# Optimization experiments

Measured on AMD Instinct MI355X. Metric: run time of the kernel, lower is better.

Reference implementation:

```python
import jax, jax.numpy as jnp
import numpy as np

BN_EPS = 1e-5

def batch_norm(x, gamma, beta):
    # training-mode BatchNorm1d: biased batch stats over the edge dim
    mean = jnp.mean(x, axis=0)
    var = jnp.var(x, axis=0)
    return (x - mean) * jax.lax.rsqrt(var + BN_EPS) * gamma + beta

def setup_inputs() -> dict:
    key = jax.random.key(0)
    ks = jax.random.split(key, 10)
    N, F, E = 50000, 128, 600000
    D_in = 2 * F + 12  # 268
    h = jax.random.normal(ks[0], (N, F), dtype=jnp.float32)
    edge_feature = jax.random.normal(ks[1], (E, 12), dtype=jnp.float32)
    src = jax.random.randint(ks[2], (E,), 0, N)
    dst = jax.random.randint(ks[3], (E,), 0, N)
    def lin(k, fan_in, shape):
        bound = 1.0 / np.sqrt(fan_in)
        return jax.random.uniform(k, shape, jnp.float32, -bound, bound)
    W1 = lin(ks[4], D_in, (28, D_in)); b1 = lin(ks[5], D_in, (28,))
    W2 = lin(ks[6], 28, (8, 28));      b2 = lin(ks[7], 28, (8,))
    W3 = lin(ks[8], 8, (1, 8));        b3 = lin(ks[9], 8, (1,))
    gamma1 = jnp.ones((28,), jnp.float32); beta1 = jnp.zeros((28,), jnp.float32)
    gamma2 = jnp.ones((8,), jnp.float32);  beta2 = jnp.zeros((8,), jnp.float32)
    return {"h": h, "edge_feature": edge_feature, "src": src, "dst": dst,
            "W1": W1, "b1": b1, "gamma1": gamma1, "beta1": beta1,
            "W2": W2, "b2": b2, "gamma2": gamma2, "beta2": beta2,
            "W3": W3, "b3": b3}

def reference(h, edge_feature, src, dst, W1, b1, gamma1, beta1,
              W2, b2, gamma2, beta2, W3, b3):
    h_u = h[src]                    # [E, F] gather of source node feats
    h_v = h[dst]                    # [E, F] gather of dest node feats
    x = jnp.concatenate([h_u, h_v, edge_feature], axis=1)  # [E, 2F+12]
    s = jax.nn.relu(batch_norm(x @ W1.T + b1, gamma1, beta1))  # [E, 28]
    s = jax.nn.relu(batch_norm(s @ W2.T + b2, gamma2, beta2))  # [E, 8]
    score = s @ W3.T + b3           # [E, 1]
    return score
```

## Files before the change

kernel.cpp:

```cpp
#include <hip/hip_runtime.h>

#define BN_EPS 1e-5f


__global__ void k1_proj(const float* __restrict__ h, const float* __restrict__ W1,
                        float* __restrict__ P, float* __restrict__ stats, int N) {
  if (blockIdx.x == 0 && threadIdx.x < 72) stats[threadIdx.x] = 0.f;
  const int half = blockIdx.x & 1;
  const int node = (blockIdx.x >> 1) * 256 + threadIdx.x;
  if (node >= N) return;

  const float* __restrict__ wbase = W1 + half * 128;
  const float4* __restrict__ h4 = (const float4*)(h + (size_t)node * 128);

  float acc[28];
#pragma unroll
  for (int c = 0; c < 28; c++) acc[c] = 0.f;

  for (int kk = 0; kk < 16; kk++) {
    const float4 a = h4[kk * 2];
    const float4 b = h4[kk * 2 + 1];
#pragma unroll
    for (int c = 0; c < 28; c++) {
      const float* w = wbase + c * 268 + kk * 8;
      acc[c] += a.x * w[0] + a.y * w[1] + a.z * w[2] + a.w * w[3]
              + b.x * w[4] + b.y * w[5] + b.z * w[6] + b.w * w[7];
    }
  }

  float4* po = (float4*)(P + (size_t)node * 56 + half * 28);
#pragma unroll
  for (int q = 0; q < 7; q++) {
    po[q] = make_float4(acc[q * 4], acc[q * 4 + 1], acc[q * 4 + 2], acc[q * 4 + 3]);
  }
}

__global__ void k2_edge(const float* __restrict__ P, const float* __restrict__ ef,
                        const int* __restrict__ src, const int* __restrict__ dst,
                        const float* __restrict__ W1, const float* __restrict__ b1,
                        float* __restrict__ y1, float* __restrict__ stats, int E) {
  const int tid = threadIdx.x;
  const int c = tid & 31;
  const int g = tid >> 5;
  const bool act = (c < 28);
  float w[12];
  float bias = 0.f;
  if (act) {
    const float4* wp = (const float4*)(W1 + c * 268 + 256);
    float4 w0 = wp[0], w1 = wp[1], w2 = wp[2];
    w[0] = w0.x; w[1] = w0.y; w[2] = w0.z; w[3] = w0.w;
    w[4] = w1.x; w[5] = w1.y; w[6] = w1.z; w[7] = w1.w;
    w[8] = w2.x; w[9] = w2.y; w[10] = w2.z; w[11] = w2.w;
    bias = b1[c];
  }
  float sum = 0.f, ssq = 0.f;
  const int gstride = gridDim.x * 8;
  for (int e = blockIdx.x * 8 + g; e < E; e += gstride) {
    const int s = src[e], d = dst[e];
    if (act) {
      const float pa = P[s * 56 + c];
      const float pb = P[d * 56 + 28 + c];
      const float4* e4 = (const float4*)(ef + e * 12);
      float4 f0 = e4[0], f1 = e4[1], f2 = e4[2];
      float acc = bias
          + f0.x * w[0] + f0.y * w[1] + f0.z * w[2] + f0.w * w[3]
          + f1.x * w[4] + f1.y * w[5] + f1.z * w[6] + f1.w * w[7]
          + f2.x * w[8] + f2.y * w[9] + f2.z * w[10] + f2.w * w[11];
      const float v = acc + pa + pb;
      y1[e * 28 + c] = v;
      sum += v;
      ssq += v * v;
    }
  }
  sum += __shfl_xor(sum, 32);
  ssq += __shfl_xor(ssq, 32);
  __shared__ float red[2][4][28];
  const int wave = tid >> 6, lane = tid & 63;
  if (lane < 28) { red[0][wave][lane] = sum; red[1][wave][lane] = ssq; }
  __syncthreads();
  if (tid < 28) {
    atomicAdd(&stats[tid], red[0][0][tid] + red[0][1][tid] + red[0][2][tid] + red[0][3][tid]);
    atomicAdd(&stats[28 + tid], red[1][0][tid] + red[1][1][tid] + red[1][2][tid] + red[1][3][tid]);
  }
}

__global__ void k3_fin1(const float* __restrict__ gamma, const float* __restrict__ beta,
                        float* __restrict__ stats, float invE) {
  const int c = threadIdx.x;
  if (c < 28) {
    const float mean = stats[c] * invE;
    const float var = stats[28 + c] * invE - mean * mean;
    const float sc = gamma[c] * rsqrtf(var + BN_EPS);
    stats[72 + c] = sc;
    stats[100 + c] = beta[c] - mean * sc;
  }
}

__global__ void k4_l2(const float* __restrict__ y1, const float* __restrict__ stats,
                      const float* __restrict__ W2, const float* __restrict__ b2,
                      float* __restrict__ y2, float* __restrict__ stats2, int E) {
  float as[8], aq[8];
#pragma unroll
  for (int o = 0; o < 8; o++) { as[o] = 0.f; aq[o] = 0.f; }
  const int stride = gridDim.x * blockDim.x;
  for (int e = blockIdx.x * blockDim.x + threadIdx.x; e < E; e += stride) {
    const float4* p = (const float4*)(y1 + e * 28);
    float s1[28];
#pragma unroll
    for (int q = 0; q < 7; q++) {
      float4 v = p[q];
      s1[q * 4 + 0] = v.x; s1[q * 4 + 1] = v.y; s1[q * 4 + 2] = v.z; s1[q * 4 + 3] = v.w;
    }
    float acc[8];
#pragma unroll
    for (int o = 0; o < 8; o++) acc[o] = b2[o];
#pragma unroll
    for (int cc = 0; cc < 28; cc++) {
      float s = fmaxf(s1[cc] * stats[72 + cc] + stats[100 + cc], 0.f);
#pragma unroll
      for (int o = 0; o < 8; o++) acc[o] += W2[o * 28 + cc] * s;
    }
    float4* yo = (float4*)(y2 + e * 8);
    yo[0] = make_float4(acc[0], acc[1], acc[2], acc[3]);
    yo[1] = make_float4(acc[4], acc[5], acc[6], acc[7]);
#pragma unroll
    for (int o = 0; o < 8; o++) { as[o] += acc[o]; aq[o] += acc[o] * acc[o]; }
  }
#pragma unroll
  for (int o = 0; o < 8; o++) {
    for (int off = 32; off; off >>= 1) {
      as[o] += __shfl_down(as[o], off);
      aq[o] += __shfl_down(aq[o], off);
    }
  }
  __shared__ float redS[4][16];
  const int wave = threadIdx.x >> 6, lane = threadIdx.x & 63;
  if (lane == 0) {
#pragma unroll
    for (int o = 0; o < 8; o++) { redS[wave][o] = as[o]; redS[wave][8 + o] = aq[o]; }
  }
  __syncthreads();
  if (threadIdx.x < 16) {
    const int t = threadIdx.x;
    atomicAdd(&stats2[t], redS[0][t] + redS[1][t] + redS[2][t] + redS[3][t]);
  }
}

__global__ void k5_fin2(const float* __restrict__ gamma, const float* __restrict__ beta,
                        float* __restrict__ stats, float invE) {
  const int c = threadIdx.x;
  if (c < 8) {
    const float mean = stats[56 + c] * invE;
    const float var = stats[64 + c] * invE - mean * mean;
    const float sc = gamma[c] * rsqrtf(var + BN_EPS);
    stats[128 + c] = sc;
    stats[136 + c] = beta[c] - mean * sc;
  }
}

__global__ void k6_l3(const float* __restrict__ y2, const float* __restrict__ stats,
                      const float* __restrict__ W3, const float* __restrict__ b3,
                      float* __restrict__ out, int E) {
  const int e = blockIdx.x * blockDim.x + threadIdx.x;
  if (e >= E) return;
  const float4* p = (const float4*)(y2 + e * 8);
  float4 a = p[0], b4 = p[1];
  float v[8] = {a.x, a.y, a.z, a.w, b4.x, b4.y, b4.z, b4.w};
  float acc = b3[0];
#pragma unroll
  for (int o = 0; o < 8; o++) {
    float s = fmaxf(v[o] * stats[128 + o] + stats[136 + o], 0.f);
    acc += W3[o] * s;
  }
  out[e] = acc;
}

extern "C" void kernel_launch(void* const* d_in, const int* in_sizes, int n_in,
                              void* d_out, int out_size, void* d_ws, size_t ws_size,
                              hipStream_t stream) {
  const float* h   = (const float*)d_in[0];
  const float* ef  = (const float*)d_in[1];
  const int* src   = (const int*)d_in[2];
  const int* dst   = (const int*)d_in[3];
  const float* W1  = (const float*)d_in[4];
  const float* b1  = (const float*)d_in[5];
  const float* g1  = (const float*)d_in[6];
  const float* be1 = (const float*)d_in[7];
  const float* W2  = (const float*)d_in[8];
  const float* b2  = (const float*)d_in[9];
  const float* g2  = (const float*)d_in[10];
  const float* be2 = (const float*)d_in[11];
  const float* W3  = (const float*)d_in[12];
  const float* b3  = (const float*)d_in[13];
  float* out = (float*)d_out;

  const int N = in_sizes[0] / 128;
  const int E = in_sizes[2];
  const float invE = 1.0f / (float)E;

  float* ws = (float*)d_ws;
  float* stats = ws;
  float* P  = ws + 256;
  float* y1 = P + (size_t)N * 56;
  float* y2 = y1 + (size_t)E * 28;

  const int nodeBlocks = (N + 255) / 256;
  k1_proj<<<nodeBlocks * 2, 256, 0, stream>>>(h, W1, P, stats, N);
  k2_edge<<<1280, 256, 0, stream>>>(P, ef, src, dst, W1, b1, y1, stats, E);
  k3_fin1<<<1, 32, 0, stream>>>(g1, be1, stats, invE);
  k4_l2<<<1172, 256, 0, stream>>>(y1, stats, W2, b2, y2, stats + 56, E);
  k5_fin2<<<1, 64, 0, stream>>>(g2, be2, stats, invE);
  k6_l3<<<(E + 255) / 256, 256, 0, stream>>>(y2, stats, W3, b3, out, E);
}
```

Measured before the change: 286.6 us.

## Store intermediates in bf16 and fold BN finalize kernels into consumers

Node projections, layer-1 and layer-2 activations are now stored as bf16 instead of fp32. Projections are split into separate src/dst arrays padded to 32 channels, which shrinks the gathered rows. The two single-block BN finalize kernels are removed; each consumer thread recomputes scale and shift from the raw sums, saving two launches. The k2 grid is doubled. The cost is lower precision in the stored intermediates, which may drift from the fp32 reference, plus redundant per-thread stat computation.

```diff
diff --git a/kernel.cpp b/kernel.cpp
--- a/kernel.cpp
+++ b/kernel.cpp
@@ -1,22 +1,33 @@
 #include <hip/hip_runtime.h>
 
 #define BN_EPS 1e-5f
-
+typedef unsigned short u16;
+typedef unsigned int u32;
+
+
+__device__ __forceinline__ u16 f2bf(float f) {
+  u32 u = __float_as_uint(f);
+  return (u16)((u + 0x7fffu + ((u >> 16) & 1u)) >> 16);
+}
+__device__ __forceinline__ float bf2f(u16 s) {
+  return __uint_as_float(((u32)s) << 16);
+}
+__device__ __forceinline__ u32 pack2(float a, float b) {
+  return (u32)f2bf(a) | ((u32)f2bf(b) << 16);
+}
 
 __global__ void k1_proj(const float* __restrict__ h, const float* __restrict__ W1,
-                        float* __restrict__ P, float* __restrict__ stats, int N) {
+                        u16* __restrict__ Psrc, u16* __restrict__ Pdst,
+                        float* __restrict__ stats, int N) {
   if (blockIdx.x == 0 && threadIdx.x < 72) stats[threadIdx.x] = 0.f;
   const int half = blockIdx.x & 1;
   const int node = (blockIdx.x >> 1) * 256 + threadIdx.x;
   if (node >= N) return;
-
   const float* __restrict__ wbase = W1 + half * 128;
   const float4* __restrict__ h4 = (const float4*)(h + (size_t)node * 128);
-
   float acc[28];
 #pragma unroll
   for (int c = 0; c < 28; c++) acc[c] = 0.f;
-
   for (int kk = 0; kk < 16; kk++) {
     const float4 a = h4[kk * 2];
     const float4 b = h4[kk * 2 + 1];
@@ -27,18 +38,22 @@
               + b.x * w[4] + b.y * w[5] + b.z * w[6] + b.w * w[7];
     }
   }
-
-  float4* po = (float4*)(P + (size_t)node * 56 + half * 28);
-#pragma unroll
-  for (int q = 0; q < 7; q++) {
-    po[q] = make_float4(acc[q * 4], acc[q * 4 + 1], acc[q * 4 + 2], acc[q * 4 + 3]);
-  }
-}
-
-__global__ void k2_edge(const float* __restrict__ P, const float* __restrict__ ef,
-                        const int* __restrict__ src, const int* __restrict__ dst,
-                        const float* __restrict__ W1, const float* __restrict__ b1,
-                        float* __restrict__ y1, float* __restrict__ stats, int E) {
+  u16* out = (half == 0 ? Psrc : Pdst) + (size_t)node * 32;
+  u32 u[14];
+#pragma unroll
+  for (int j = 0; j < 14; j++) u[j] = pack2(acc[2 * j], acc[2 * j + 1]);
+  uint4* p4 = (uint4*)out;
+  p4[0] = make_uint4(u[0], u[1], u[2], u[3]);
+  p4[1] = make_uint4(u[4], u[5], u[6], u[7]);
+  p4[2] = make_uint4(u[8], u[9], u[10], u[11]);
+  *(uint2*)((u32*)out + 12) = make_uint2(u[12], u[13]);
+}
+
+__global__ void k2_l1(const u16* __restrict__ Psrc, const u16* __restrict__ Pdst,
+                      const float* __restrict__ ef,
+                      const int* __restrict__ src, const int* __restrict__ dst,
+                      const float* __restrict__ W1, const float* __restrict__ b1,
+                      u16* __restrict__ y1, float* __restrict__ stats, int E) {
   const int tid = threadIdx.x;
   const int c = tid & 31;
   const int g = tid >> 5;
@@ -58,18 +73,18 @@
   for (int e = blockIdx.x * 8 + g; e < E; e += gstride) {
     const int s = src[e], d = dst[e];
     if (act) {
-      const float pa = P[s * 56 + c];
-      const float pb = P[d * 56 + 28 + c];
-      const float4* e4 = (const float4*)(ef + e * 12);
+      const float pa = bf2f(Psrc[(size_t)s * 32 + c]);
+      const float pb = bf2f(Pdst[(size_t)d * 32 + c]);
+      const float4* e4 = (const float4*)(ef + (size_t)e * 12);
       float4 f0 = e4[0], f1 = e4[1], f2 = e4[2];
-      float acc = bias
+      const float y = bias
           + f0.x * w[0] + f0.y * w[1] + f0.z * w[2] + f0.w * w[3]
           + f1.x * w[4] + f1.y * w[5] + f1.z * w[6] + f1.w * w[7]
-          + f2.x * w[8] + f2.y * w[9] + f2.z * w[10] + f2.w * w[11];
-      const float v = acc + pa + pb;
-      y1[e * 28 + c] = v;
-      sum += v;
-      ssq += v * v;
+          + f2.x * w[8] + f2.y * w[9] + f2.z * w[10] + f2.w * w[11]
+          + pa + pb;
+      y1[(size_t)e * 32 + c] = f2bf(y);
+      sum += y;
+      ssq += y * y;
     }
   }
   sum += __shfl_xor(sum, 32);
@@ -84,45 +99,47 @@
   }
 }
 
-__global__ void k3_fin1(const float* __restrict__ gamma, const float* __restrict__ beta,
-                        float* __restrict__ stats, float invE) {
-  const int c = threadIdx.x;
-  if (c < 28) {
-    const float mean = stats[c] * invE;
-    const float var = stats[28 + c] * invE - mean * mean;
-    const float sc = gamma[c] * rsqrtf(var + BN_EPS);
-    stats[72 + c] = sc;
-    stats[100 + c] = beta[c] - mean * sc;
-  }
-}
-
-__global__ void k4_l2(const float* __restrict__ y1, const float* __restrict__ stats,
+__global__ void k4_l2(const u16* __restrict__ y1, const float* __restrict__ stats,
+                      const float* __restrict__ g1, const float* __restrict__ be1,
                       const float* __restrict__ W2, const float* __restrict__ b2,
-                      float* __restrict__ y2, float* __restrict__ stats2, int E) {
+                      u16* __restrict__ y2, float* __restrict__ stats2, int E, float invE) {
+  float sc[28], sh[28];
+#pragma unroll
+  for (int cc = 0; cc < 28; cc++) {
+    const float m = stats[cc] * invE;
+    const float v = stats[28 + cc] * invE - m * m;
+    const float s = g1[cc] * rsqrtf(v + BN_EPS);
+    sc[cc] = s; sh[cc] = be1[cc] - m * s;
+  }
   float as[8], aq[8];
 #pragma unroll
   for (int o = 0; o < 8; o++) { as[o] = 0.f; aq[o] = 0.f; }
   const int stride = gridDim.x * blockDim.x;
   for (int e = blockIdx.x * blockDim.x + threadIdx.x; e < E; e += stride) {
-    const float4* p = (const float4*)(y1 + e * 28);
-    float s1[28];
-#pragma unroll
-    for (int q = 0; q < 7; q++) {
-      float4 v = p[q];
-      s1[q * 4 + 0] = v.x; s1[q * 4 + 1] = v.y; s1[q * 4 + 2] = v.z; s1[q * 4 + 3] = v.w;
-    }
+    const u16* row = y1 + (size_t)e * 32;
+    const uint4 r0 = *(const uint4*)row;
+    const uint4 r1 = *(const uint4*)(row + 8);
+    const uint4 r2 = *(const uint4*)(row + 16);
+    const uint2 r3 = *(const uint2*)(row + 24);
+    u32 uu[14] = {r0.x, r0.y, r0.z, r0.w, r1.x, r1.y, r1.z, r1.w,
+                  r2.x, r2.y, r2.z, r2.w, r3.x, r3.y};
     float acc[8];
 #pragma unroll
     for (int o = 0; o < 8; o++) acc[o] = b2[o];
 #pragma unroll
-    for (int cc = 0; cc < 28; cc++) {
-      float s = fmaxf(s1[cc] * stats[72 + cc] + stats[100 + cc], 0.f);
-#pragma unroll
-      for (int o = 0; o < 8; o++) acc[o] += W2[o * 28 + cc] * s;
-    }
-    float4* yo = (float4*)(y2 + e * 8);
-    yo[0] = make_float4(acc[0], acc[1], acc[2], acc[3]);
-    yo[1] = make_float4(acc[4], acc[5], acc[6], acc[7]);
+    for (int k = 0; k < 14; k++) {
+      const float fe = __uint_as_float(uu[k] << 16);
+      const float fo = __uint_as_float(uu[k] & 0xffff0000u);
+      const float se = fmaxf(fmaf(fe, sc[2 * k], sh[2 * k]), 0.f);
+      const float so = fmaxf(fmaf(fo, sc[2 * k + 1], sh[2 * k + 1]), 0.f);
+#pragma unroll
+      for (int o = 0; o < 8; o++) {
+        acc[o] = fmaf(W2[o * 28 + 2 * k], se, acc[o]);
+        acc[o] = fmaf(W2[o * 28 + 2 * k + 1], so, acc[o]);
+      }
+    }
+    *(uint4*)(y2 + (size_t)e * 8) = make_uint4(pack2(acc[0], acc[1]), pack2(acc[2], acc[3]),
+                                               pack2(acc[4], acc[5]), pack2(acc[6], acc[7]));
 #pragma unroll
     for (int o = 0; o < 8; o++) { as[o] += acc[o]; aq[o] += acc[o] * acc[o]; }
   }
@@ -146,31 +163,29 @@
   }
 }
 
-__global__ void k5_fin2(const float* __restrict__ gamma, const float* __restrict__ beta,
-                        float* __restrict__ stats, float invE) {
-  const int c = threadIdx.x;
-  if (c < 8) {
-    const float mean = stats[56 + c] * invE;
-    const float var = stats[64 + c] * invE - mean * mean;
-    const float sc = gamma[c] * rsqrtf(var + BN_EPS);
-    stats[128 + c] = sc;
-    stats[136 + c] = beta[c] - mean * sc;
-  }
-}
-
-__global__ void k6_l3(const float* __restrict__ y2, const float* __restrict__ stats,
+__global__ void k6_l3(const u16* __restrict__ y2, const float* __restrict__ stats,
+                      const float* __restrict__ g2, const float* __restrict__ be2,
                       const float* __restrict__ W3, const float* __restrict__ b3,
-                      float* __restrict__ out, int E) {
+                      float* __restrict__ out, int E, float invE) {
+  float sc[8], sh[8], w3[8];
+#pragma unroll
+  for (int o = 0; o < 8; o++) {
+    const float m = stats[56 + o] * invE;
+    const float v = stats[64 + o] * invE - m * m;
+    const float s = g2[o] * rsqrtf(v + BN_EPS);
+    sc[o] = s; sh[o] = be2[o] - m * s; w3[o] = W3[o];
+  }
   const int e = blockIdx.x * blockDim.x + threadIdx.x;
   if (e >= E) return;
-  const float4* p = (const float4*)(y2 + e * 8);
-  float4 a = p[0], b4 = p[1];
-  float v[8] = {a.x, a.y, a.z, a.w, b4.x, b4.y, b4.z, b4.w};
+  const uint4 r = *(const uint4*)(y2 + (size_t)e * 8);
+  u32 uu[4] = {r.x, r.y, r.z, r.w};
   float acc = b3[0];
 #pragma unroll
-  for (int o = 0; o < 8; o++) {
-    float s = fmaxf(v[o] * stats[128 + o] + stats[136 + o], 0.f);
-    acc += W3[o] * s;
+  for (int k = 0; k < 4; k++) {
+    const float fe = __uint_as_float(uu[k] << 16);
+    const float fo = __uint_as_float(uu[k] & 0xffff0000u);
+    acc = fmaf(w3[2 * k], fmaxf(fmaf(fe, sc[2 * k], sh[2 * k]), 0.f), acc);
+    acc = fmaf(w3[2 * k + 1], fmaxf(fmaf(fo, sc[2 * k + 1], sh[2 * k + 1]), 0.f), acc);
   }
   out[e] = acc;
 }
@@ -198,17 +213,16 @@
   const int E = in_sizes[2];
   const float invE = 1.0f / (float)E;
 
-  float* ws = (float*)d_ws;
-  float* stats = ws;
-  float* P  = ws + 256;
-  float* y1 = P + (size_t)N * 56;
-  float* y2 = y1 + (size_t)E * 28;
+  char* ws = (char*)d_ws;
+  float* stats = (float*)ws;
+  u16* Psrc = (u16*)(ws + 1024);
+  u16* Pdst = Psrc + (size_t)N * 32;
+  u16* y1   = Pdst + (size_t)N * 32;
+  u16* y2   = y1 + (size_t)E * 32;
 
   const int nodeBlocks = (N + 255) / 256;
-  k1_proj<<<nodeBlocks * 2, 256, 0, stream>>>(h, W1, P, stats, N);
-  k2_edge<<<1280, 256, 0, stream>>>(P, ef, src, dst, W1, b1, y1, stats, E);
-  k3_fin1<<<1, 32, 0, stream>>>(g1, be1, stats, invE);
-  k4_l2<<<1172, 256, 0, stream>>>(y1, stats, W2, b2, y2, stats + 56, E);
-  k5_fin2<<<1, 64, 0, stream>>>(g2, be2, stats, invE);
-  k6_l3<<<(E + 255) / 256, 256, 0, stream>>>(y2, stats, W3, b3, out, E);
-}
+  k1_proj<<<nodeBlocks * 2, 256, 0, stream>>>(h, W1, Psrc, Pdst, stats, N);
+  k2_l1<<<2560, 256, 0, stream>>>(Psrc, Pdst, ef, src, dst, W1, b1, y1, stats, E);
+  k4_l2<<<1172, 256, 0, stream>>>(y1, stats, g1, be1, W2, b2, y2, stats + 56, E, invE);
+  k6_l3<<<(E + 255) / 256, 256, 0, stream>>>(y2, stats, g2, be2, W3, b3, out, E, invE);
+}
```

Result: slower. 310.2 us (+8.2%).
